# Optimization experiments

Measured on AMD Instinct MI355X. Metric: run time of the kernel, lower is better.

## Reference

```python
import jax, jax.numpy as jnp
import numpy as np

IOU_THRESHOLD = 0.5
NEG_POS_RATIO = 3
VAR0, VAR1 = 0.1, 0.2  # SSD encoding variances


def _make_boxes(key, shape, lo_c, hi_c, lo_s, hi_s):
    k1, k2 = jax.random.split(key)
    c = jax.random.uniform(k1, shape + (2,), minval=lo_c, maxval=hi_c)
    s = jax.random.uniform(k2, shape + (2,), minval=lo_s, maxval=hi_s)
    return jnp.concatenate([c - s / 2, c + s / 2], axis=-1)  # [xmin,ymin,xmax,ymax], w,h > 0


def setup_inputs() -> dict:
    B, P, C, M = 64, 24564, 21, 50
    key = jax.random.key(0)
    k1, k2, k3, k4, k5 = jax.random.split(key, 5)
    loc_preds = jax.random.normal(k1, (B, P, 4), dtype=jnp.float32) * 0.1
    conf_preds = jax.random.normal(k2, (B, P, C), dtype=jnp.float32)
    default_boxes = _make_boxes(k3, (P,), 0.1, 0.9, 0.05, 0.25)
    gt_boxes = _make_boxes(k4, (B, M), 0.2, 0.8, 0.05, 0.35)
    gt_labels = jax.random.randint(k5, (B, M), 1, C, dtype=jnp.int32)
    return {"loc_preds": loc_preds, "conf_preds": conf_preds, "gt_boxes": gt_boxes,
            "gt_labels": gt_labels, "default_boxes": default_boxes}


def box_iou(a, b):
    # a: (P,4), b: (M,4) corner form -> (P,M)
    lt = jnp.maximum(a[:, None, :2], b[None, :, :2])
    rb = jnp.minimum(a[:, None, 2:], b[None, :, 2:])
    wh = jnp.clip(rb - lt, 0.0)
    inter = wh[..., 0] * wh[..., 1]
    area_a = (a[:, 2] - a[:, 0]) * (a[:, 3] - a[:, 1])
    area_b = (b[:, 2] - b[:, 0]) * (b[:, 3] - b[:, 1])
    return inter / (area_a[:, None] + area_b[None, :] - inter)


def encode_boxes(matched, default):
    g_c = (matched[:, :2] + matched[:, 2:]) / 2
    g_wh = matched[:, 2:] - matched[:, :2]
    d_c = (default[:, :2] + default[:, 2:]) / 2
    d_wh = default[:, 2:] - default[:, :2]
    dxy = (g_c - d_c) / (VAR0 * d_wh)
    dwh = jnp.log(g_wh / d_wh) / VAR1
    return jnp.concatenate([dxy, dwh], axis=1)  # (P,4)


def reference(loc_preds, conf_preds, gt_boxes, gt_labels, default_boxes):
    P = default_boxes.shape[0]
    M = gt_boxes.shape[1]

    def match_one(truths, labels):
        ious = box_iou(default_boxes, truths)                 # (P,M)
        best_truth_iou = ious.max(axis=1)                     # (P,)
        best_truth_idx = ious.argmax(axis=1)                  # (P,)
        best_prior_idx = ious.argmax(axis=0)                  # (M,)
        best_truth_iou = best_truth_iou.at[best_prior_idx].set(1.0)
        best_truth_idx = best_truth_idx.at[best_prior_idx].set(jnp.arange(M))
        matches = truths[best_truth_idx]                      # (P,4)
        conf = jnp.where(best_truth_iou < IOU_THRESHOLD, 0, labels[best_truth_idx])
        return encode_boxes(matches, default_boxes), conf

    loc_t, conf_t = jax.vmap(match_one)(gt_boxes, gt_labels)  # (B,P,4), (B,P)

    pos_mask = conf_t > 0
    num_pos = jnp.maximum(pos_mask.sum(), 1)

    # Smooth L1 (beta=1), summed over positive priors
    diff = jnp.abs(loc_preds - loc_t)
    sl1 = jnp.where(diff < 1.0, 0.5 * diff * diff, diff - 0.5)
    loc_loss = jnp.sum(sl1 * pos_mask[..., None].astype(sl1.dtype))

    # per-prior cross entropy
    logp = jax.nn.log_softmax(conf_preds, axis=-1)            # (B,P,C)
    ce_all = -jnp.take_along_axis(logp, conf_t[..., None].astype(jnp.int32), axis=-1)[..., 0]

    # hard negative mining: double-argsort rank trick
    ce_neg = jnp.where(pos_mask, 0.0, ce_all)
    order = jnp.argsort(-ce_neg, axis=1)
    rank = jnp.argsort(order, axis=1)
    num_neg = NEG_POS_RATIO * pos_mask.sum(axis=1, keepdims=True)
    neg_mask = rank < num_neg
    conf_mask = pos_mask | neg_mask
    conf_loss = jnp.sum(ce_all * conf_mask.astype(ce_all.dtype))

    return (loc_loss + conf_loss) / num_pos.astype(jnp.float32)
```

## Files before the change

### kernel.cpp

```cpp
#include <hip/hip_runtime.h>
#include <cstdint>


static constexpr int NPB    = 256;
static constexpr int KC     = 21;
static constexpr int MAXM   = 64;
static constexpr int FORCED = 0x40000000;

typedef unsigned int       u32;
typedef unsigned long long u64;

#define GLOAD_LDS16(gp, lp)                                                        \
  __builtin_amdgcn_global_load_lds((const __attribute__((address_space(1))) u32*)(gp), \
                                   (__attribute__((address_space(3))) u32*)(lp), 16, 0, 0)

__global__ __launch_bounds__(256)
void k_matchA(const float4* __restrict__ dbox, const float4* __restrict__ gbox,
              int* __restrict__ bt_code, int P, int M) {
    int b = blockIdx.y;
    int t = threadIdx.x;
    int p = blockIdx.x * NPB + t;
    __shared__ float4 sg[MAXM];
    __shared__ float  sga[MAXM];
    if (t < M) {
        float4 g = gbox[b * M + t];
        sg[t]  = g;
        sga[t] = (g.z - g.x) * (g.w - g.y);
    }
    __syncthreads();
    if (p >= P) return;
    float4 d = dbox[p];
    float ad = (d.z - d.x) * (d.w - d.y);
    float bi = 0.f, bu = 1.f;
    int bm = 0;
    for (int m = 0; m < M; ++m) {
        float4 g = sg[m];
        float lx = fmaxf(d.x, g.x), ly = fmaxf(d.y, g.y);
        float rx = fminf(d.z, g.z), ry = fminf(d.w, g.w);
        float w = fmaxf(rx - lx, 0.f), h = fmaxf(ry - ly, 0.f);
        float inter = w * h;
        float uni = ad + sga[m] - inter;
        if (inter * bu > bi * uni) { bi = inter; bu = uni; bm = m; }
    }
    bt_code[(size_t)b * P + p] = (2.f * bi >= bu) ? bm : -1;
}

__global__ __launch_bounds__(256)
void k_argmaxB(const float4* __restrict__ dbox, const float4* __restrict__ gbox,
               int* __restrict__ bp_idx, int P, int M) {
    int b  = blockIdx.y;
    int m0 = blockIdx.x * 2;
    int t  = threadIdx.x;
    bool two = (m0 + 1) < M;
    float4 g0 = gbox[b * M + m0];
    float4 g1 = two ? gbox[b * M + m0 + 1] : g0;
    float ga0 = (g0.z - g0.x) * (g0.w - g0.y);
    float ga1 = (g1.z - g1.x) * (g1.w - g1.y);
    float bi0 = 0.f, bu0 = 1.f, bi1 = 0.f, bu1 = 1.f;
    int bp0 = 0x7FFFFFFF, bp1 = 0x7FFFFFFF;
    for (int p = t; p < P; p += NPB) {
        float4 d = dbox[p];
        float ad = (d.z - d.x) * (d.w - d.y);
        {
            float lx = fmaxf(d.x, g0.x), ly = fmaxf(d.y, g0.y);
            float rx = fminf(d.z, g0.z), ry = fminf(d.w, g0.w);
            float w = fmaxf(rx - lx, 0.f), h = fmaxf(ry - ly, 0.f);
            float inter = w * h;
            float uni = ad + ga0 - inter;
            float l = inter * bu0, r = bi0 * uni;
            if (l > r || (l == r && p < bp0)) { bi0 = inter; bu0 = uni; bp0 = p; }
        }
        {
            float lx = fmaxf(d.x, g1.x), ly = fmaxf(d.y, g1.y);
            float rx = fminf(d.z, g1.z), ry = fminf(d.w, g1.w);
            float w = fmaxf(rx - lx, 0.f), h = fmaxf(ry - ly, 0.f);
            float inter = w * h;
            float uni = ad + ga1 - inter;
            float l = inter * bu1, r = bi1 * uni;
            if (l > r || (l == r && p < bp1)) { bi1 = inter; bu1 = uni; bp1 = p; }
        }
    }
    #pragma unroll
    for (int o = 32; o; o >>= 1) {
        float oi0 = __shfl_xor(bi0, o), ou0 = __shfl_xor(bu0, o);
        int   op0 = __shfl_xor(bp0, o);
        float l0 = oi0 * bu0, r0 = bi0 * ou0;
        if (l0 > r0 || (l0 == r0 && op0 < bp0)) { bi0 = oi0; bu0 = ou0; bp0 = op0; }
        float oi1 = __shfl_xor(bi1, o), ou1 = __shfl_xor(bu1, o);
        int   op1 = __shfl_xor(bp1, o);
        float l1 = oi1 * bu1, r1 = bi1 * ou1;
        if (l1 > r1 || (l1 == r1 && op1 < bp1)) { bi1 = oi1; bu1 = ou1; bp1 = op1; }
    }
    __shared__ float wi[2][4], wu[2][4];
    __shared__ int   wp[2][4];
    int wid = t >> 6;
    if ((t & 63) == 0) {
        wi[0][wid] = bi0; wu[0][wid] = bu0; wp[0][wid] = bp0;
        wi[1][wid] = bi1; wu[1][wid] = bu1; wp[1][wid] = bp1;
    }
    __syncthreads();
    if (t == 0) {
        #pragma unroll
        for (int w = 1; w < 4; ++w) {
            float l = wi[0][w] * bu0, r = bi0 * wu[0][w];
            if (l > r || (l == r && wp[0][w] < bp0)) { bi0 = wi[0][w]; bu0 = wu[0][w]; bp0 = wp[0][w]; }
        }
        bp_idx[b * M + m0] = bp0;
        if (two) {
            #pragma unroll
            for (int w = 1; w < 4; ++w) {
                float l = wi[1][w] * bu1, r = bi1 * wu[1][w];
                if (l > r || (l == r && wp[1][w] < bp1)) { bi1 = wi[1][w]; bu1 = wu[1][w]; bp1 = wp[1][w]; }
            }
            bp_idx[b * M + m0 + 1] = bp1;
        }
    }
}

__global__ __launch_bounds__(256)
void k_force2(const int* __restrict__ bp_idx, int* __restrict__ bt_code, int P, int M, int BM) {
    int i = blockIdx.x * blockDim.x + threadIdx.x;
    if (i >= BM) return;
    int b = i / M, m = i - b * M;
    int p = bp_idx[i];
    atomicMax(&bt_code[(size_t)b * P + p], FORCED + m);
}

__global__ __launch_bounds__(256)
void k_loss(const float* __restrict__ conf, const float4* __restrict__ locp,
            const float4* __restrict__ dbox, const float4* __restrict__ gbox,
            const int* __restrict__ glab, const int* __restrict__ bt_code,
            float* __restrict__ ce_neg, float2* __restrict__ partials,
            int* __restrict__ poscnt, int P, int M) {
    int b  = blockIdx.y;
    int t  = threadIdx.x;
    int p0 = blockIdx.x * NPB;
    int npr = min(NPB, P - p0);
    __shared__ float slog[NPB * KC];
    const float* src = conf + ((size_t)b * P + p0) * KC;
    int nbytes = npr * KC * 4;
    int wave = t >> 6, lane = t & 63;
    int nfull = nbytes >> 10;
    for (int j = wave; j < nfull; j += 4) {
        int boff = __builtin_amdgcn_readfirstlane(j << 10);
        const float* g = src + (boff >> 2) + lane * 4;
        GLOAD_LDS16(g, (char*)slog + boff);
    }
    int rem16 = (nbytes & 1023) >> 4;
    if (wave == 0 && lane < rem16) {
        int boff = __builtin_amdgcn_readfirstlane(nfull << 10);
        const float* g = src + (boff >> 2) + lane * 4;
        GLOAD_LDS16(g, (char*)slog + boff);
    }
    int donew = (nfull << 8) + (rem16 << 2);
    for (int i = donew + t; i < (nbytes >> 2); i += NPB) slog[i] = src[i];
    __syncthreads();

    float sl1 = 0.f, cep = 0.f, posf = 0.f;
    if (t < npr) {
        int p = p0 + t;
        int code = bt_code[(size_t)b * P + p];
        bool pos = code >= 0;
        int  mi  = (code >= FORCED) ? (code - FORCED) : code;
        const float* L = slog + t * KC;
        float v[KC];
        #pragma unroll
        for (int c = 0; c < KC; ++c) v[c] = L[c];
        float mx = v[0];
        #pragma unroll
        for (int c = 1; c < KC; ++c) mx = fmaxf(mx, v[c]);
        float s = 0.f;
        #pragma unroll
        for (int c = 0; c < KC; ++c) s += __expf(v[c] - mx);
        int lab = pos ? glab[b * M + mi] : 0;
        float ce = mx + __logf(s) - L[lab];
        ce_neg[(size_t)b * P + p] = pos ? 0.f : ce;
        if (pos) {
            posf = 1.f;
            cep  = ce;
            float4 g = gbox[b * M + mi];
            float4 d = dbox[p];
            float gw = g.z - g.x, gh = g.w - g.y;
            float dw = d.z - d.x, dh = d.w - d.y;
            float e0 = (0.5f * (g.x + g.z) - 0.5f * (d.x + d.z)) / (0.1f * dw);
            float e1 = (0.5f * (g.y + g.w) - 0.5f * (d.y + d.w)) / (0.1f * dh);
            float e2 = __logf(gw / dw) * 5.0f;
            float e3 = __logf(gh / dh) * 5.0f;
            float4 lp = locp[(size_t)b * P + p];
            float d0 = fabsf(lp.x - e0), d1 = fabsf(lp.y - e1);
            float d2 = fabsf(lp.z - e2), d3 = fabsf(lp.w - e3);
            sl1  = (d0 < 1.f ? 0.5f * d0 * d0 : d0 - 0.5f);
            sl1 += (d1 < 1.f ? 0.5f * d1 * d1 : d1 - 0.5f);
            sl1 += (d2 < 1.f ? 0.5f * d2 * d2 : d2 - 0.5f);
            sl1 += (d3 < 1.f ? 0.5f * d3 * d3 : d3 - 0.5f);
        }
    }
    #pragma unroll
    for (int o = 32; o; o >>= 1) {
        sl1  += __shfl_down(sl1, o);
        cep  += __shfl_down(cep, o);
        posf += __shfl_down(posf, o);
    }
    __shared__ float red[3][4];
    int wid = t >> 6;
    if ((t & 63) == 0) { red[0][wid] = sl1; red[1][wid] = cep; red[2][wid] = posf; }
    __syncthreads();
    if (t == 0) {
        float A  = red[0][0] + red[0][1] + red[0][2] + red[0][3];
        float Cc = red[1][0] + red[1][1] + red[1][2] + red[1][3];
        float Pp = red[2][0] + red[2][1] + red[2][2] + red[2][3];
        int blk = blockIdx.y * gridDim.x + blockIdx.x;
        partials[blk] = make_float2(A, Cc);
        poscnt[blk]   = (int)(Pp + 0.5f);
    }
}

__global__ __launch_bounds__(1024)
void k_select(const float* __restrict__ ce_neg, const int* __restrict__ poscnt,
              int* __restrict__ row_pos, float* __restrict__ negsum, int P, int NBX) {
    const int NT = 1024, NW = 16;
    int b = blockIdx.x, t = threadIdx.x;
    int wid = t >> 6;
    __shared__ int hist[NW][256];
    __shared__ int sscan[256];
    __shared__ u32 s_prefix;
    __shared__ int s_krem;
    __shared__ int s_k;
    __shared__ float wsum[16];

    {
        int c = 0;
        for (int i = t; i < NBX; i += NT) c += poscnt[b * NBX + i];
        #pragma unroll
        for (int o = 32; o; o >>= 1) c += __shfl_down(c, o);
        if ((t & 63) == 0) ((int*)wsum)[wid] = c;
        __syncthreads();
        if (t == 0) {
            int s = 0;
            #pragma unroll
            for (int i = 0; i < NW; ++i) s += ((int*)wsum)[i];
            s_k = s;
            row_pos[b] = s;
        }
        __syncthreads();
    }
    int k = 3 * s_k;

    const float*  row  = ce_neg + (size_t)b * P;
    const float4* row4 = (const float4*)row;
    int P4 = P >> 2;
    u32 thr;
    if (k <= 0) {
        thr = 0xFFFFFFFFu;
    } else if (k >= P) {
        thr = 0u;
    } else {
        if (t == 0) { s_prefix = 0u; s_krem = k; }
        for (int d = 3; d >= 0; --d) {
            for (int i = t; i < NW * 256; i += NT) ((int*)hist)[i] = 0;
            __syncthreads();
            u32 pre  = s_prefix;
            int krem = s_krem;
            u32 maskhi = (d == 3) ? 0u : (0xFFFFFFFFu << ((d + 1) * 8));
            int sh = 8 * d;
            int* h = hist[wid];
            for (int q = t; q < P4; q += NT) {
                float4 v = row4[q];
                u32 w0 = __float_as_uint(v.x), w1 = __float_as_uint(v.y);
                u32 w2 = __float_as_uint(v.z), w3 = __float_as_uint(v.w);
                if ((w0 & maskhi) == pre) atomicAdd(&h[(w0 >> sh) & 255], 1);
                if ((w1 & maskhi) == pre) atomicAdd(&h[(w1 >> sh) & 255], 1);
                if ((w2 & maskhi) == pre) atomicAdd(&h[(w2 >> sh) & 255], 1);
                if ((w3 & maskhi) == pre) atomicAdd(&h[(w3 >> sh) & 255], 1);
            }
            __syncthreads();
            if (t < 256) {
                int c = 0;
                #pragma unroll
                for (int w = 0; w < NW; ++w) c += hist[w][t];
                sscan[t] = c;
            }
            __syncthreads();
            for (int off = 1; off < 256; off <<= 1) {
                int x = 0;
                if (t < 256) { x = sscan[t]; if (t + off < 256) x += sscan[t + off]; }
                __syncthreads();
                if (t < 256) sscan[t] = x;
                __syncthreads();
            }
            if (t < 256) {
                int S  = sscan[t];
                int Sn = (t < 255) ? sscan[t + 1] : 0;
                if (S >= krem && Sn < krem) {
                    s_prefix = pre | ((u32)t << sh);
                    s_krem   = krem - Sn;
                }
            }
            __syncthreads();
        }
        thr = s_prefix;
    }
    float partial = 0.f;
    for (int q = t; q < P4; q += NT) {
        float4 v = row4[q];
        if (__float_as_uint(v.x) >= thr) partial += v.x;
        if (__float_as_uint(v.y) >= thr) partial += v.y;
        if (__float_as_uint(v.z) >= thr) partial += v.z;
        if (__float_as_uint(v.w) >= thr) partial += v.w;
    }
    #pragma unroll
    for (int o = 32; o; o >>= 1) partial += __shfl_down(partial, o);
    __syncthreads();
    if ((t & 63) == 0) wsum[wid] = partial;
    __syncthreads();
    if (t == 0) {
        float s = 0.f;
        #pragma unroll
        for (int i = 0; i < 16; ++i) s += wsum[i];
        negsum[b] = s;
    }
}

__global__ __launch_bounds__(256)
void k_final(const float2* __restrict__ partials, const int* __restrict__ row_pos,
             const float* __restrict__ negsum, int nblk, int B, float* __restrict__ out) {
    int t = threadIdx.x;
    double a = 0.0, c = 0.0;
    for (int i = t; i < nblk; i += 256) {
        float2 p = partials[i];
        a += (double)p.x;
        c += (double)p.y;
    }
    double ns = 0.0;
    int np = 0;
    for (int i = t; i < B; i += 256) { ns += (double)negsum[i]; np += row_pos[i]; }
    #pragma unroll
    for (int o = 32; o; o >>= 1) {
        a  += __shfl_down(a, o);
        c  += __shfl_down(c, o);
        ns += __shfl_down(ns, o);
        np += __shfl_down(np, o);
    }
    __shared__ double red[3][4];
    __shared__ int    redn[4];
    int wid = t >> 6;
    if ((t & 63) == 0) { red[0][wid] = a; red[1][wid] = c; red[2][wid] = ns; redn[wid] = np; }
    __syncthreads();
    if (t == 0) {
        double A = red[0][0] + red[0][1] + red[0][2] + red[0][3];
        double C = red[1][0] + red[1][1] + red[1][2] + red[1][3];
        double N = red[2][0] + red[2][1] + red[2][2] + red[2][3];
        int    P_ = redn[0] + redn[1] + redn[2] + redn[3];
        if (P_ < 1) P_ = 1;
        out[0] = (float)((A + C + N) / (double)P_);
    }
}

extern "C" void kernel_launch(void* const* d_in, const int* in_sizes, int n_in,
                              void* d_out, int out_size, void* d_ws, size_t ws_size,
                              hipStream_t stream) {
    const float* loc_preds     = (const float*)d_in[0];
    const float* conf_preds    = (const float*)d_in[1];
    const float* gt_boxes      = (const float*)d_in[2];
    const int*   gt_labels     = (const int*)d_in[3];
    const float* default_boxes = (const float*)d_in[4];

    int P = in_sizes[4] / 4;
    int B = in_sizes[0] / (P * 4);
    int M = in_sizes[3] / B;
    int BM  = B * M;
    int NBX = (P + NPB - 1) / NPB;
    int nblk = NBX * B;

    char* w = (char*)d_ws;
    float2* partials = (float2*)w;             w += (size_t)nblk * sizeof(float2);
    int*    poscnt   = (int*)w;                w += (size_t)nblk * sizeof(int);
    int*    row_pos  = (int*)w;                w += (size_t)B * sizeof(int);
    float*  negsum   = (float*)w;              w += (size_t)B * sizeof(float);
    int*    bp_idx   = (int*)w;                w += (size_t)BM * sizeof(int);
    int*    bt_code  = (int*)w;                w += (size_t)B * P * 4;
    float*  ce_neg   = (float*)w;              w += (size_t)B * P * 4;

    dim3 g1(NBX, B);
    k_matchA<<<g1, NPB, 0, stream>>>((const float4*)default_boxes, (const float4*)gt_boxes,
                                     bt_code, P, M);
    dim3 g2((M + 1) / 2, B);
    k_argmaxB<<<g2, NPB, 0, stream>>>((const float4*)default_boxes, (const float4*)gt_boxes,
                                      bp_idx, P, M);
    k_force2<<<(BM + 255) / 256, 256, 0, stream>>>(bp_idx, bt_code, P, M, BM);
    k_loss<<<g1, NPB, 0, stream>>>(conf_preds, (const float4*)loc_preds,
                                   (const float4*)default_boxes, (const float4*)gt_boxes,
                                   gt_labels, bt_code, ce_neg, partials, poscnt, P, M);
    k_select<<<B, 1024, 0, stream>>>(ce_neg, poscnt, row_pos, negsum, P, NBX);
    k_final<<<1, 256, 0, stream>>>(partials, row_pos, negsum, nblk, B, (float*)d_out);
}
```

Before: 345.9 us.

## Fuse per-prior and per-truth IoU argmax into one matching kernel; trim radix-select histograms

```diff
diff --git a/kernel.cpp b/kernel.cpp
--- a/kernel.cpp
+++ b/kernel.cpp
@@ -15,115 +15,83 @@
                                    (__attribute__((address_space(3))) u32*)(lp), 16, 0, 0)
 
 __global__ __launch_bounds__(256)
-void k_matchA(const float4* __restrict__ dbox, const float4* __restrict__ gbox,
-              int* __restrict__ bt_code, int P, int M) {
-    int b = blockIdx.y;
-    int t = threadIdx.x;
+void k_match(const float4* __restrict__ dbox, const float4* __restrict__ gbox,
+             int* __restrict__ bt_code, u64* __restrict__ cand, int P, int M, int NBX) {
+    int b = blockIdx.y, t = threadIdx.x;
     int p = blockIdx.x * NPB + t;
     __shared__ float4 sg[MAXM];
     __shared__ float  sga[MAXM];
+    __shared__ float  siou[NPB][51];
+    __shared__ float  sqv[4][64];
+    __shared__ int    sqp[4][64];
     if (t < M) {
         float4 g = gbox[b * M + t];
         sg[t]  = g;
         sga[t] = (g.z - g.x) * (g.w - g.y);
     }
     __syncthreads();
-    if (p >= P) return;
-    float4 d = dbox[p];
-    float ad = (d.z - d.x) * (d.w - d.y);
-    float bi = 0.f, bu = 1.f;
-    int bm = 0;
-    for (int m = 0; m < M; ++m) {
-        float4 g = sg[m];
-        float lx = fmaxf(d.x, g.x), ly = fmaxf(d.y, g.y);
-        float rx = fminf(d.z, g.z), ry = fminf(d.w, g.w);
-        float w = fmaxf(rx - lx, 0.f), h = fmaxf(ry - ly, 0.f);
-        float inter = w * h;
-        float uni = ad + sga[m] - inter;
-        if (inter * bu > bi * uni) { bi = inter; bu = uni; bm = m; }
-    }
-    bt_code[(size_t)b * P + p] = (2.f * bi >= bu) ? bm : -1;
-}
-
-__global__ __launch_bounds__(256)
-void k_argmaxB(const float4* __restrict__ dbox, const float4* __restrict__ gbox,
-               int* __restrict__ bp_idx, int P, int M) {
-    int b  = blockIdx.y;
-    int m0 = blockIdx.x * 2;
-    int t  = threadIdx.x;
-    bool two = (m0 + 1) < M;
-    float4 g0 = gbox[b * M + m0];
-    float4 g1 = two ? gbox[b * M + m0 + 1] : g0;
-    float ga0 = (g0.z - g0.x) * (g0.w - g0.y);
-    float ga1 = (g1.z - g1.x) * (g1.w - g1.y);
-    float bi0 = 0.f, bu0 = 1.f, bi1 = 0.f, bu1 = 1.f;
-    int bp0 = 0x7FFFFFFF, bp1 = 0x7FFFFFFF;
-    for (int p = t; p < P; p += NPB) {
+
+    if (p < P) {
         float4 d = dbox[p];
         float ad = (d.z - d.x) * (d.w - d.y);
-        {
-            float lx = fmaxf(d.x, g0.x), ly = fmaxf(d.y, g0.y);
-            float rx = fminf(d.z, g0.z), ry = fminf(d.w, g0.w);
+        float bv = -1.f; int bm = 0;
+        for (int m = 0; m < M; ++m) {
+            float4 g = sg[m];
+            float lx = fmaxf(d.x, g.x), ly = fmaxf(d.y, g.y);
+            float rx = fminf(d.z, g.z), ry = fminf(d.w, g.w);
             float w = fmaxf(rx - lx, 0.f), h = fmaxf(ry - ly, 0.f);
             float inter = w * h;
-            float uni = ad + ga0 - inter;
-            float l = inter * bu0, r = bi0 * uni;
-            if (l > r || (l == r && p < bp0)) { bi0 = inter; bu0 = uni; bp0 = p; }
-        }
-        {
-            float lx = fmaxf(d.x, g1.x), ly = fmaxf(d.y, g1.y);
-            float rx = fminf(d.z, g1.z), ry = fminf(d.w, g1.w);
-            float w = fmaxf(rx - lx, 0.f), h = fmaxf(ry - ly, 0.f);
-            float inter = w * h;
-            float uni = ad + ga1 - inter;
-            float l = inter * bu1, r = bi1 * uni;
-            if (l > r || (l == r && p < bp1)) { bi1 = inter; bu1 = uni; bp1 = p; }
-        }
-    }
-    #pragma unroll
-    for (int o = 32; o; o >>= 1) {
-        float oi0 = __shfl_xor(bi0, o), ou0 = __shfl_xor(bu0, o);
-        int   op0 = __shfl_xor(bp0, o);
-        float l0 = oi0 * bu0, r0 = bi0 * ou0;
-        if (l0 > r0 || (l0 == r0 && op0 < bp0)) { bi0 = oi0; bu0 = ou0; bp0 = op0; }
-        float oi1 = __shfl_xor(bi1, o), ou1 = __shfl_xor(bu1, o);
-        int   op1 = __shfl_xor(bp1, o);
-        float l1 = oi1 * bu1, r1 = bi1 * ou1;
-        if (l1 > r1 || (l1 == r1 && op1 < bp1)) { bi1 = oi1; bu1 = ou1; bp1 = op1; }
-    }
-    __shared__ float wi[2][4], wu[2][4];
-    __shared__ int   wp[2][4];
-    int wid = t >> 6;
-    if ((t & 63) == 0) {
-        wi[0][wid] = bi0; wu[0][wid] = bu0; wp[0][wid] = bp0;
-        wi[1][wid] = bi1; wu[1][wid] = bu1; wp[1][wid] = bp1;
-    }
-    __syncthreads();
-    if (t == 0) {
-        #pragma unroll
-        for (int w = 1; w < 4; ++w) {
-            float l = wi[0][w] * bu0, r = bi0 * wu[0][w];
-            if (l > r || (l == r && wp[0][w] < bp0)) { bi0 = wi[0][w]; bu0 = wu[0][w]; bp0 = wp[0][w]; }
-        }
-        bp_idx[b * M + m0] = bp0;
-        if (two) {
-            #pragma unroll
-            for (int w = 1; w < 4; ++w) {
-                float l = wi[1][w] * bu1, r = bi1 * wu[1][w];
-                if (l > r || (l == r && wp[1][w] < bp1)) { bi1 = wi[1][w]; bu1 = wu[1][w]; bp1 = wp[1][w]; }
-            }
-            bp_idx[b * M + m0 + 1] = bp1;
-        }
+            float uni = ad + sga[m] - inter;
+            float v = __fdividef(inter, uni);
+            siou[t][m] = v;
+            if (v > bv) { bv = v; bm = m; }
+        }
+        bt_code[(size_t)b * P + p] = (bv >= 0.5f) ? bm : -1;
+    } else {
+        for (int m = 0; m < M; ++m) siou[t][m] = -2.f;
+    }
+    __syncthreads();
+
+    int q = t >> 6, m = t & 63;
+    if (m < M) {
+        float best = -3.f; int bj = 0;
+        int rbase = q * 64;
+        #pragma unroll 8
+        for (int j = 0; j < 64; ++j) {
+            float v = siou[rbase + j][m];
+            if (v > best) { best = v; bj = j; }
+        }
+        sqv[q][m] = best;
+        sqp[q][m] = blockIdx.x * NPB + rbase + bj;
+    }
+    __syncthreads();
+    if (t < M) {
+        float bv2 = -3.f; int bp2 = 0;
+        #pragma unroll
+        for (int qq = 0; qq < 4; ++qq) {
+            float v = sqv[qq][t];
+            if (v > bv2) { bv2 = v; bp2 = sqp[qq][t]; }
+        }
+        if (bv2 < 0.f) bv2 = 0.f;
+        cand[((size_t)b * M + t) * NBX + blockIdx.x] =
+            ((u64)__float_as_uint(bv2) << 32) | (u32)bp2;
     }
 }
 
 __global__ __launch_bounds__(256)
-void k_force2(const int* __restrict__ bp_idx, int* __restrict__ bt_code, int P, int M, int BM) {
-    int i = blockIdx.x * blockDim.x + threadIdx.x;
+void k_reduce_force(const u64* __restrict__ cand, int* __restrict__ bt_code,
+                    int P, int M, int BM, int NBX) {
+    int i = blockIdx.x * 256 + threadIdx.x;
     if (i >= BM) return;
+    const u64* cc = cand + (size_t)i * NBX;
+    u32 bh = 0, bp = 0;
+    for (int j = 0; j < NBX; ++j) {
+        u64 kk = cc[j];
+        u32 hi = (u32)(kk >> 32);
+        if (hi > bh) { bh = hi; bp = (u32)kk; }
+    }
     int b = i / M, m = i - b * M;
-    int p = bp_idx[i];
-    atomicMax(&bt_code[(size_t)b * P + p], FORCED + m);
+    atomicMax(&bt_code[(size_t)b * P + (int)bp], FORCED + m);
 }
 
 __global__ __launch_bounds__(256)
@@ -218,36 +186,32 @@
 __global__ __launch_bounds__(1024)
 void k_select(const float* __restrict__ ce_neg, const int* __restrict__ poscnt,
               int* __restrict__ row_pos, float* __restrict__ negsum, int P, int NBX) {
-    const int NT = 1024, NW = 16;
-    int b = blockIdx.x, t = threadIdx.x;
-    int wid = t >> 6;
-    __shared__ int hist[NW][256];
-    __shared__ int sscan[256];
-    __shared__ u32 s_prefix;
-    __shared__ int s_krem;
-    __shared__ int s_k;
+    const int NT = 1024;
+    int b = blockIdx.x, t = threadIdx.x, lane = t & 63, wid = t >> 6;
+    __shared__ int   hist[4][256];
+    __shared__ int   ired[16];
     __shared__ float wsum[16];
+    __shared__ u32   s_prefix;
+    __shared__ int   s_krem, s_k;
 
     {
         int c = 0;
         for (int i = t; i < NBX; i += NT) c += poscnt[b * NBX + i];
         #pragma unroll
         for (int o = 32; o; o >>= 1) c += __shfl_down(c, o);
-        if ((t & 63) == 0) ((int*)wsum)[wid] = c;
+        if (lane == 0) ired[wid] = c;
         __syncthreads();
         if (t == 0) {
             int s = 0;
             #pragma unroll
-            for (int i = 0; i < NW; ++i) s += ((int*)wsum)[i];
-            s_k = s;
-            row_pos[b] = s;
+            for (int i2 = 0; i2 < 16; ++i2) s += ired[i2];
+            s_k = s; row_pos[b] = s;
+            s_prefix = 0u; s_krem = 3 * s;
         }
         __syncthreads();
     }
     int k = 3 * s_k;
-
-    const float*  row  = ce_neg + (size_t)b * P;
-    const float4* row4 = (const float4*)row;
+    const float4* row4 = (const float4*)(ce_neg + (size_t)b * P);
     int P4 = P >> 2;
     u32 thr;
     if (k <= 0) {
@@ -255,54 +219,65 @@
     } else if (k >= P) {
         thr = 0u;
     } else {
-        if (t == 0) { s_prefix = 0u; s_krem = k; }
         for (int d = 3; d >= 0; --d) {
-            for (int i = t; i < NW * 256; i += NT) ((int*)hist)[i] = 0;
+            for (int i = t; i < 4 * 256; i += NT) ((int*)hist)[i] = 0;
             __syncthreads();
             u32 pre  = s_prefix;
             int krem = s_krem;
             u32 maskhi = (d == 3) ? 0u : (0xFFFFFFFFu << ((d + 1) * 8));
             int sh = 8 * d;
-            int* h = hist[wid];
-            for (int q = t; q < P4; q += NT) {
-                float4 v = row4[q];
-                u32 w0 = __float_as_uint(v.x), w1 = __float_as_uint(v.y);
-                u32 w2 = __float_as_uint(v.z), w3 = __float_as_uint(v.w);
-                if ((w0 & maskhi) == pre) atomicAdd(&h[(w0 >> sh) & 255], 1);
-                if ((w1 & maskhi) == pre) atomicAdd(&h[(w1 >> sh) & 255], 1);
-                if ((w2 & maskhi) == pre) atomicAdd(&h[(w2 >> sh) & 255], 1);
-                if ((w3 & maskhi) == pre) atomicAdd(&h[(w3 >> sh) & 255], 1);
-            }
-            __syncthreads();
-            if (t < 256) {
-                int c = 0;
+            int* h = hist[wid & 3];
+            for (int qq = t; qq < P4; qq += NT) {
+                float4 v = row4[qq];
+                u32 wv0 = __float_as_uint(v.x), wv1 = __float_as_uint(v.y);
+                u32 wv2 = __float_as_uint(v.z), wv3 = __float_as_uint(v.w);
                 #pragma unroll
-                for (int w = 0; w < NW; ++w) c += hist[w][t];
-                sscan[t] = c;
-            }
-            __syncthreads();
-            for (int off = 1; off < 256; off <<= 1) {
-                int x = 0;
-                if (t < 256) { x = sscan[t]; if (t + off < 256) x += sscan[t + off]; }
-                __syncthreads();
-                if (t < 256) sscan[t] = x;
-                __syncthreads();
-            }
-            if (t < 256) {
-                int S  = sscan[t];
-                int Sn = (t < 255) ? sscan[t + 1] : 0;
-                if (S >= krem && Sn < krem) {
-                    s_prefix = pre | ((u32)t << sh);
-                    s_krem   = krem - Sn;
+                for (int j = 0; j < 4; ++j) {
+                    u32 wb = (j == 0) ? wv0 : (j == 1) ? wv1 : (j == 2) ? wv2 : wv3;
+                    bool valid = (wb & maskhi) == pre;
+                    int bin = (int)((wb >> sh) & 255u);
+                    if (d == 3) {
+                        u64 todo = __ballot(valid);
+                        while (todo) {
+                            int l  = __builtin_ctzll(todo);
+                            int bb = __shfl(bin, l);
+                            u64 same = __ballot(valid && (bin == bb));
+                            if (lane == l) atomicAdd(&h[bb], (int)__builtin_popcountll(same));
+                            todo &= ~same;
+                        }
+                    } else if (valid) {
+                        atomicAdd(&h[bin], 1);
+                    }
                 }
             }
             __syncthreads();
+            if (wid == 0) {
+                int v0 = 4 * lane;
+                int c0 = hist[0][v0]     + hist[1][v0]     + hist[2][v0]     + hist[3][v0];
+                int c1 = hist[0][v0 + 1] + hist[1][v0 + 1] + hist[2][v0 + 1] + hist[3][v0 + 1];
+                int c2 = hist[0][v0 + 2] + hist[1][v0 + 2] + hist[2][v0 + 2] + hist[3][v0 + 2];
+                int c3 = hist[0][v0 + 3] + hist[1][v0 + 3] + hist[2][v0 + 3] + hist[3][v0 + 3];
+                int sl = c0 + c1 + c2 + c3;
+                int T = sl;
+                #pragma unroll
+                for (int o = 1; o < 64; o <<= 1) {
+                    int x = __shfl_down(T, o);
+                    if (lane + o < 64) T += x;
+                }
+                int Tn = T - sl;
+                int S3 = Tn + c3, S2 = S3 + c2, S1 = S2 + c1, S0 = S1 + c0;
+                if (S0 >= krem && S1 < krem) { s_prefix = pre | ((u32)(v0    ) << sh); s_krem = krem - S1; }
+                if (S1 >= krem && S2 < krem) { s_prefix = pre | ((u32)(v0 + 1) << sh); s_krem = krem - S2; }
+                if (S2 >= krem && S3 < krem) { s_prefix = pre | ((u32)(v0 + 2) << sh); s_krem = krem - S3; }
+                if (S3 >= krem && Tn < krem) { s_prefix = pre | ((u32)(v0 + 3) << sh); s_krem = krem - Tn; }
+            }
+            __syncthreads();
         }
         thr = s_prefix;
     }
     float partial = 0.f;
-    for (int q = t; q < P4; q += NT) {
-        float4 v = row4[q];
+    for (int qq = t; qq < P4; qq += NT) {
+        float4 v = row4[qq];
         if (__float_as_uint(v.x) >= thr) partial += v.x;
         if (__float_as_uint(v.y) >= thr) partial += v.y;
         if (__float_as_uint(v.z) >= thr) partial += v.z;
@@ -311,7 +286,7 @@
     #pragma unroll
     for (int o = 32; o; o >>= 1) partial += __shfl_down(partial, o);
     __syncthreads();
-    if ((t & 63) == 0) wsum[wid] = partial;
+    if (lane == 0) wsum[wid] = partial;
     __syncthreads();
     if (t == 0) {
         float s = 0.f;
@@ -377,17 +352,15 @@
     int*    poscnt   = (int*)w;                w += (size_t)nblk * sizeof(int);
     int*    row_pos  = (int*)w;                w += (size_t)B * sizeof(int);
     float*  negsum   = (float*)w;              w += (size_t)B * sizeof(float);
-    int*    bp_idx   = (int*)w;                w += (size_t)BM * sizeof(int);
+    w = (char*)(((uintptr_t)w + 7) & ~(uintptr_t)7);
+    u64*    cand     = (u64*)w;                w += (size_t)BM * NBX * sizeof(u64);
     int*    bt_code  = (int*)w;                w += (size_t)B * P * 4;
     float*  ce_neg   = (float*)w;              w += (size_t)B * P * 4;
 
     dim3 g1(NBX, B);
-    k_matchA<<<g1, NPB, 0, stream>>>((const float4*)default_boxes, (const float4*)gt_boxes,
-                                     bt_code, P, M);
-    dim3 g2((M + 1) / 2, B);
-    k_argmaxB<<<g2, NPB, 0, stream>>>((const float4*)default_boxes, (const float4*)gt_boxes,
-                                      bp_idx, P, M);
-    k_force2<<<(BM + 255) / 256, 256, 0, stream>>>(bp_idx, bt_code, P, M, BM);
+    k_match<<<g1, NPB, 0, stream>>>((const float4*)default_boxes, (const float4*)gt_boxes,
+                                    bt_code, cand, P, M, NBX);
+    k_reduce_force<<<(BM + 255) / 256, 256, 0, stream>>>(cand, bt_code, P, M, BM, NBX);
     k_loss<<<g1, NPB, 0, stream>>>(conf_preds, (const float4*)loc_preds,
                                    (const float4*)default_boxes, (const float4*)gt_boxes,
                                    gt_labels, bt_code, ce_neg, partials, poscnt, P, M);
```

Measured after the change: 353.0 us. 1.02x slower.

## Use 3-pass 11-bit radix select and four GT boxes per argmax block

Applied to the files above, without the earlier changes.

```diff
diff --git a/kernel.cpp b/kernel.cpp
--- a/kernel.cpp
+++ b/kernel.cpp
@@ -49,70 +49,59 @@
 void k_argmaxB(const float4* __restrict__ dbox, const float4* __restrict__ gbox,
                int* __restrict__ bp_idx, int P, int M) {
     int b  = blockIdx.y;
-    int m0 = blockIdx.x * 2;
+    int m0 = blockIdx.x * 4;
     int t  = threadIdx.x;
-    bool two = (m0 + 1) < M;
-    float4 g0 = gbox[b * M + m0];
-    float4 g1 = two ? gbox[b * M + m0 + 1] : g0;
-    float ga0 = (g0.z - g0.x) * (g0.w - g0.y);
-    float ga1 = (g1.z - g1.x) * (g1.w - g1.y);
-    float bi0 = 0.f, bu0 = 1.f, bi1 = 0.f, bu1 = 1.f;
-    int bp0 = 0x7FFFFFFF, bp1 = 0x7FFFFFFF;
+    int nm = min(4, M - m0);
+    float4 g[4]; float ga[4], bi[4], bu[4]; int bp[4];
+    #pragma unroll
+    for (int j = 0; j < 4; ++j) {
+        int mm = m0 + ((j < nm) ? j : (nm - 1));
+        g[j]  = gbox[b * M + mm];
+        ga[j] = (g[j].z - g[j].x) * (g[j].w - g[j].y);
+        bi[j] = 0.f; bu[j] = 1.f; bp[j] = 0x7FFFFFFF;
+    }
     for (int p = t; p < P; p += NPB) {
         float4 d = dbox[p];
         float ad = (d.z - d.x) * (d.w - d.y);
-        {
-            float lx = fmaxf(d.x, g0.x), ly = fmaxf(d.y, g0.y);
-            float rx = fminf(d.z, g0.z), ry = fminf(d.w, g0.w);
+        #pragma unroll
+        for (int j = 0; j < 4; ++j) {
+            float lx = fmaxf(d.x, g[j].x), ly = fmaxf(d.y, g[j].y);
+            float rx = fminf(d.z, g[j].z), ry = fminf(d.w, g[j].w);
             float w = fmaxf(rx - lx, 0.f), h = fmaxf(ry - ly, 0.f);
             float inter = w * h;
-            float uni = ad + ga0 - inter;
-            float l = inter * bu0, r = bi0 * uni;
-            if (l > r || (l == r && p < bp0)) { bi0 = inter; bu0 = uni; bp0 = p; }
-        }
-        {
-            float lx = fmaxf(d.x, g1.x), ly = fmaxf(d.y, g1.y);
-            float rx = fminf(d.z, g1.z), ry = fminf(d.w, g1.w);
-            float w = fmaxf(rx - lx, 0.f), h = fmaxf(ry - ly, 0.f);
-            float inter = w * h;
-            float uni = ad + ga1 - inter;
-            float l = inter * bu1, r = bi1 * uni;
-            if (l > r || (l == r && p < bp1)) { bi1 = inter; bu1 = uni; bp1 = p; }
+            float uni = ad + ga[j] - inter;
+            float l = inter * bu[j], r = bi[j] * uni;
+            if (l > r || (l == r && p < bp[j])) { bi[j] = inter; bu[j] = uni; bp[j] = p; }
         }
     }
     #pragma unroll
     for (int o = 32; o; o >>= 1) {
-        float oi0 = __shfl_xor(bi0, o), ou0 = __shfl_xor(bu0, o);
-        int   op0 = __shfl_xor(bp0, o);
-        float l0 = oi0 * bu0, r0 = bi0 * ou0;
-        if (l0 > r0 || (l0 == r0 && op0 < bp0)) { bi0 = oi0; bu0 = ou0; bp0 = op0; }
-        float oi1 = __shfl_xor(bi1, o), ou1 = __shfl_xor(bu1, o);
-        int   op1 = __shfl_xor(bp1, o);
-        float l1 = oi1 * bu1, r1 = bi1 * ou1;
-        if (l1 > r1 || (l1 == r1 && op1 < bp1)) { bi1 = oi1; bu1 = ou1; bp1 = op1; }
-    }
-    __shared__ float wi[2][4], wu[2][4];
-    __shared__ int   wp[2][4];
+        #pragma unroll
+        for (int j = 0; j < 4; ++j) {
+            float oi = __shfl_xor(bi[j], o), ou = __shfl_xor(bu[j], o);
+            int   op = __shfl_xor(bp[j], o);
+            float l = oi * bu[j], r = bi[j] * ou;
+            if (l > r || (l == r && op < bp[j])) { bi[j] = oi; bu[j] = ou; bp[j] = op; }
+        }
+    }
+    __shared__ float wi[4][4], wu[4][4];
+    __shared__ int   wp[4][4];
     int wid = t >> 6;
     if ((t & 63) == 0) {
-        wi[0][wid] = bi0; wu[0][wid] = bu0; wp[0][wid] = bp0;
-        wi[1][wid] = bi1; wu[1][wid] = bu1; wp[1][wid] = bp1;
+        #pragma unroll
+        for (int j = 0; j < 4; ++j) { wi[j][wid] = bi[j]; wu[j][wid] = bu[j]; wp[j][wid] = bp[j]; }
     }
     __syncthreads();
     if (t == 0) {
         #pragma unroll
-        for (int w = 1; w < 4; ++w) {
-            float l = wi[0][w] * bu0, r = bi0 * wu[0][w];
-            if (l > r || (l == r && wp[0][w] < bp0)) { bi0 = wi[0][w]; bu0 = wu[0][w]; bp0 = wp[0][w]; }
-        }
-        bp_idx[b * M + m0] = bp0;
-        if (two) {
+        for (int j = 0; j < 4; ++j) {
+            float ci = bi[j], cu = bu[j]; int cp = bp[j];
             #pragma unroll
             for (int w = 1; w < 4; ++w) {
-                float l = wi[1][w] * bu1, r = bi1 * wu[1][w];
-                if (l > r || (l == r && wp[1][w] < bp1)) { bi1 = wi[1][w]; bu1 = wu[1][w]; bp1 = wp[1][w]; }
-            }
-            bp_idx[b * M + m0 + 1] = bp1;
+                float l = wi[j][w] * cu, r = ci * wu[j][w];
+                if (l > r || (l == r && wp[j][w] < cp)) { ci = wi[j][w]; cu = wu[j][w]; cp = wp[j][w]; }
+            }
+            if (j < nm) bp_idx[b * M + m0 + j] = cp;
         }
     }
 }
@@ -143,14 +132,14 @@
     int nfull = nbytes >> 10;
     for (int j = wave; j < nfull; j += 4) {
         int boff = __builtin_amdgcn_readfirstlane(j << 10);
-        const float* g = src + (boff >> 2) + lane * 4;
-        GLOAD_LDS16(g, (char*)slog + boff);
+        const float* gp = src + (boff >> 2) + lane * 4;
+        GLOAD_LDS16(gp, (char*)slog + boff);
     }
     int rem16 = (nbytes & 1023) >> 4;
     if (wave == 0 && lane < rem16) {
         int boff = __builtin_amdgcn_readfirstlane(nfull << 10);
-        const float* g = src + (boff >> 2) + lane * 4;
-        GLOAD_LDS16(g, (char*)slog + boff);
+        const float* gp = src + (boff >> 2) + lane * 4;
+        GLOAD_LDS16(gp, (char*)slog + boff);
     }
     int donew = (nfull << 8) + (rem16 << 2);
     for (int i = donew + t; i < (nbytes >> 2); i += NPB) slog[i] = src[i];
@@ -178,12 +167,12 @@
         if (pos) {
             posf = 1.f;
             cep  = ce;
-            float4 g = gbox[b * M + mi];
+            float4 gg = gbox[b * M + mi];
             float4 d = dbox[p];
-            float gw = g.z - g.x, gh = g.w - g.y;
+            float gw = gg.z - gg.x, gh = gg.w - gg.y;
             float dw = d.z - d.x, dh = d.w - d.y;
-            float e0 = (0.5f * (g.x + g.z) - 0.5f * (d.x + d.z)) / (0.1f * dw);
-            float e1 = (0.5f * (g.y + g.w) - 0.5f * (d.y + d.w)) / (0.1f * dh);
+            float e0 = (0.5f * (gg.x + gg.z) - 0.5f * (d.x + d.z)) / (0.1f * dw);
+            float e1 = (0.5f * (gg.y + gg.w) - 0.5f * (d.y + d.w)) / (0.1f * dh);
             float e2 = __logf(gw / dw) * 5.0f;
             float e3 = __logf(gh / dh) * 5.0f;
             float4 lp = locp[(size_t)b * P + p];
@@ -218,36 +207,33 @@
 __global__ __launch_bounds__(1024)
 void k_select(const float* __restrict__ ce_neg, const int* __restrict__ poscnt,
               int* __restrict__ row_pos, float* __restrict__ negsum, int P, int NBX) {
-    const int NT = 1024, NW = 16;
-    int b = blockIdx.x, t = threadIdx.x;
-    int wid = t >> 6;
-    __shared__ int hist[NW][256];
-    __shared__ int sscan[256];
-    __shared__ u32 s_prefix;
-    __shared__ int s_krem;
-    __shared__ int s_k;
+    const int NT = 1024, NCOPY = 4;
+    int b = blockIdx.x, t = threadIdx.x, lane = t & 63, wid = t >> 6;
+    __shared__ int   hist[NCOPY][2048];
+    __shared__ int   scn[2048];
+    __shared__ int   seg[16], seg2[16], ired[16];
     __shared__ float wsum[16];
+    __shared__ u32   s_prefix;
+    __shared__ int   s_krem, s_k;
 
     {
         int c = 0;
         for (int i = t; i < NBX; i += NT) c += poscnt[b * NBX + i];
         #pragma unroll
         for (int o = 32; o; o >>= 1) c += __shfl_down(c, o);
-        if ((t & 63) == 0) ((int*)wsum)[wid] = c;
+        if (lane == 0) ired[wid] = c;
         __syncthreads();
         if (t == 0) {
             int s = 0;
             #pragma unroll
-            for (int i = 0; i < NW; ++i) s += ((int*)wsum)[i];
-            s_k = s;
-            row_pos[b] = s;
+            for (int i2 = 0; i2 < 16; ++i2) s += ired[i2];
+            s_k = s; row_pos[b] = s;
+            s_prefix = 0u; s_krem = 3 * s;
         }
         __syncthreads();
     }
     int k = 3 * s_k;
-
-    const float*  row  = ce_neg + (size_t)b * P;
-    const float4* row4 = (const float4*)row;
+    const float4* row4 = (const float4*)(ce_neg + (size_t)b * P);
     int P4 = P >> 2;
     u32 thr;
     if (k <= 0) {
@@ -255,54 +241,70 @@
     } else if (k >= P) {
         thr = 0u;
     } else {
-        if (t == 0) { s_prefix = 0u; s_krem = k; }
-        for (int d = 3; d >= 0; --d) {
-            for (int i = t; i < NW * 256; i += NT) ((int*)hist)[i] = 0;
+        #pragma unroll
+        for (int pass = 0; pass < 3; ++pass) {
+            const int sh    = (pass == 0) ? 21 : (pass == 1) ? 10 : 0;
+            const int nbits = (pass == 2) ? 10 : 11;
+            const int nb    = 1 << nbits;
+            const u32 maskhi = (pass == 0) ? 0u : (0xFFFFFFFFu << (sh + nbits));
+            for (int i = t; i < NCOPY * 2048; i += NT) ((int*)hist)[i] = 0;
             __syncthreads();
             u32 pre  = s_prefix;
             int krem = s_krem;
-            u32 maskhi = (d == 3) ? 0u : (0xFFFFFFFFu << ((d + 1) * 8));
-            int sh = 8 * d;
-            int* h = hist[wid];
-            for (int q = t; q < P4; q += NT) {
-                float4 v = row4[q];
+            int* h = hist[wid & (NCOPY - 1)];
+            for (int qq = t; qq < P4; qq += NT) {
+                float4 v = row4[qq];
                 u32 w0 = __float_as_uint(v.x), w1 = __float_as_uint(v.y);
                 u32 w2 = __float_as_uint(v.z), w3 = __float_as_uint(v.w);
-                if ((w0 & maskhi) == pre) atomicAdd(&h[(w0 >> sh) & 255], 1);
-                if ((w1 & maskhi) == pre) atomicAdd(&h[(w1 >> sh) & 255], 1);
-                if ((w2 & maskhi) == pre) atomicAdd(&h[(w2 >> sh) & 255], 1);
-                if ((w3 & maskhi) == pre) atomicAdd(&h[(w3 >> sh) & 255], 1);
-            }
-            __syncthreads();
-            if (t < 256) {
+                if ((w0 & maskhi) == pre) atomicAdd(&h[(w0 >> sh) & (nb - 1)], 1);
+                if ((w1 & maskhi) == pre) atomicAdd(&h[(w1 >> sh) & (nb - 1)], 1);
+                if ((w2 & maskhi) == pre) atomicAdd(&h[(w2 >> sh) & (nb - 1)], 1);
+                if ((w3 & maskhi) == pre) atomicAdd(&h[(w3 >> sh) & (nb - 1)], 1);
+            }
+            __syncthreads();
+            for (int j = t; j < nb; j += NT) {
                 int c = 0;
                 #pragma unroll
-                for (int w = 0; w < NW; ++w) c += hist[w][t];
-                sscan[t] = c;
-            }
-            __syncthreads();
-            for (int off = 1; off < 256; off <<= 1) {
-                int x = 0;
-                if (t < 256) { x = sscan[t]; if (t + off < 256) x += sscan[t + off]; }
-                __syncthreads();
-                if (t < 256) sscan[t] = x;
-                __syncthreads();
-            }
-            if (t < 256) {
-                int S  = sscan[t];
-                int Sn = (t < 255) ? sscan[t + 1] : 0;
-                if (S >= krem && Sn < krem) {
-                    s_prefix = pre | ((u32)t << sh);
-                    s_krem   = krem - Sn;
-                }
+                for (int w = 0; w < NCOPY; ++w) c += hist[w][j];
+                scn[j] = c;
+            }
+            __syncthreads();
+            int sb   = nb >> 4;
+            int nper = sb >> 6;
+            int base = wid * sb + lane * nper;
+            int c0 = scn[base];
+            int c1 = (nper == 2) ? scn[base + 1] : 0;
+            int sl = c0 + c1;
+            int T = sl;
+            #pragma unroll
+            for (int o = 1; o < 64; o <<= 1) {
+                int x = __shfl_down(T, o);
+                if (lane + o < 64) T += x;
+            }
+            if (lane == 0) seg[wid] = T;
+            __syncthreads();
+            if (t < 16) {
+                int sse = 0;
+                for (int j2 = t + 1; j2 < 16; ++j2) sse += seg[j2];
+                seg2[t] = sse;
+            }
+            __syncthreads();
+            int A1 = seg2[wid] + (T - sl);
+            int S1 = A1 + c1;
+            int S0 = S1 + c0;
+            if (nper == 2) {
+                if (S0 >= krem && S1 < krem) { s_prefix = pre | ((u32)base << sh);       s_krem = krem - S1; }
+                if (S1 >= krem && A1 < krem) { s_prefix = pre | ((u32)(base + 1) << sh); s_krem = krem - A1; }
+            } else {
+                if (S0 >= krem && A1 < krem) { s_prefix = pre | ((u32)base << sh);       s_krem = krem - A1; }
             }
             __syncthreads();
         }
         thr = s_prefix;
     }
     float partial = 0.f;
-    for (int q = t; q < P4; q += NT) {
-        float4 v = row4[q];
+    for (int qq = t; qq < P4; qq += NT) {
+        float4 v = row4[qq];
         if (__float_as_uint(v.x) >= thr) partial += v.x;
         if (__float_as_uint(v.y) >= thr) partial += v.y;
         if (__float_as_uint(v.z) >= thr) partial += v.z;
@@ -311,7 +313,7 @@
     #pragma unroll
     for (int o = 32; o; o >>= 1) partial += __shfl_down(partial, o);
     __syncthreads();
-    if ((t & 63) == 0) wsum[wid] = partial;
+    if (lane == 0) wsum[wid] = partial;
     __syncthreads();
     if (t == 0) {
         float s = 0.f;
@@ -384,7 +386,7 @@
     dim3 g1(NBX, B);
     k_matchA<<<g1, NPB, 0, stream>>>((const float4*)default_boxes, (const float4*)gt_boxes,
                                      bt_code, P, M);
-    dim3 g2((M + 1) / 2, B);
+    dim3 g2((M + 3) / 4, B);
     k_argmaxB<<<g2, NPB, 0, stream>>>((const float4*)default_boxes, (const float4*)gt_boxes,
                                       bp_idx, P, M);
     k_force2<<<(BM + 255) / 256, 256, 0, stream>>>(bp_idx, bt_code, P, M, BM);
```

Result: faster. 334.0 us (-3.4%).
